# Kernel tuning notes

Hardware: AMD Instinct MI355X
Metric: run time of the kernel (lower is better)

The kernel has to match this reference:

```python
import jax, jax.numpy as jnp
import numpy as np

CHAR_EMB = 30
CHAR_HID = 100  # bidirectional -> 50 per direction
HID = CHAR_HID // 2
VOCAB = 100
B, S, T = 64, 256, 16


def setup_inputs() -> dict:
    key = jax.random.key(0)
    ks = jax.random.split(key, 10)
    char_ids = jax.random.randint(ks[0], (B, S, T), 0, VOCAB, dtype=jnp.int64)
    scale = np.sqrt(3.0 / CHAR_EMB)
    emb = jax.random.uniform(ks[1], (VOCAB, CHAR_EMB), minval=-scale, maxval=scale, dtype=jnp.float32)
    # torch LSTM param layout: w_ih [4H, in], w_hh [4H, H], gate order i,f,g,o
    k = 1.0 / np.sqrt(HID)
    def u(kk, shape):
        return jax.random.uniform(kk, shape, minval=-k, maxval=k, dtype=jnp.float32)
    return {
        "char_ids": char_ids,
        "emb": emb,
        "w_ih_f": u(ks[2], (4 * HID, CHAR_EMB)), "w_hh_f": u(ks[3], (4 * HID, HID)),
        "b_ih_f": u(ks[4], (4 * HID,)), "b_hh_f": u(ks[5], (4 * HID,)),
        "w_ih_r": u(ks[6], (4 * HID, CHAR_EMB)), "w_hh_r": u(ks[7], (4 * HID, HID)),
        "b_ih_r": u(ks[8], (4 * HID,)), "b_hh_r": u(ks[9], (4 * HID,)),
    }


def _lstm_scan(x, w_ih, w_hh, b_ih, b_hh):
    # x: [N, T, E] -> outputs ys [T, N, H], final h [N, H]
    N = x.shape[0]
    xw = jnp.einsum('nte,ge->ntg', x, w_ih) + (b_ih + b_hh)  # [N, T, 4H]
    xw = jnp.transpose(xw, (1, 0, 2))  # [T, N, 4H]

    def step(carry, xt):
        h, c = carry
        gates = xt + h @ w_hh.T
        i, f, g, o = jnp.split(gates, 4, axis=-1)
        i = jax.nn.sigmoid(i); f = jax.nn.sigmoid(f)
        g = jnp.tanh(g); o = jax.nn.sigmoid(o)
        c = f * c + i * g
        h = o * jnp.tanh(c)
        return (h, c), h

    h0 = jnp.zeros((N, HID), x.dtype)
    (hT, _), ys = jax.lax.scan(step, (h0, h0), xw)
    return ys, hT


def reference(char_ids, emb, w_ih_f, w_hh_f, b_ih_f, b_hh_f,
              w_ih_r, w_hh_r, b_ih_r, b_hh_r):
    b, s, t = char_ids.shape
    ids = char_ids.reshape(b * s, t)                 # [N, T]
    lengths = (ids != 0).sum(axis=1)                 # ragged lengths (pad id 0)
    x = emb[ids]                                     # [N, T, E]; dropout = identity (eval)

    # forward direction: need hidden at position lengths-1
    ys_f, _ = _lstm_scan(x, w_ih_f, w_hh_f, b_ih_f, b_hh_f)   # [T, N, H]
    ys_f = jnp.transpose(ys_f, (1, 0, 2))                      # [N, T, H]
    idx = jnp.maximum(lengths - 1, 0)[:, None, None]           # guard all-pad rows
    h_fwd = jnp.take_along_axis(ys_f, idx, axis=1)[:, 0, :]    # [N, H]

    # backward direction: output at t=0 == final carry of reversed scan
    _, h_bwd = _lstm_scan(x[:, ::-1, :], w_ih_r, w_hh_r, b_ih_r, b_hh_r)  # [N, H]

    out = jnp.concatenate([h_fwd, h_bwd], axis=-1)   # [N, 2H]
    return out.reshape(b, s, CHAR_HID)
```

## Files before the change

### kernel.cpp

```cpp
#include <hip/hip_runtime.h>

#define T 16
#define E 30
#define H 50
#define VOCAB 100
#define ROWS 208
#define K1 1.44269504089f
#define K2 2.88539008178f
#define NTILE 13

typedef _Float16 v8hf __attribute__((ext_vector_type(8)));
typedef float v4f __attribute__((ext_vector_type(4)));

extern "C" __device__ float __ocml_native_exp2_f32(float);
__device__ __forceinline__ float e2(float x)   { return __ocml_native_exp2_f32(x); }
__device__ __forceinline__ float rcpf(float x) { return __builtin_amdgcn_rcpf(x); }

__global__ void build_tbl(const float* __restrict__ emb,
                          const float* __restrict__ w_ih,
                          const float* __restrict__ b_ih,
                          const float* __restrict__ b_hh,
                          float* __restrict__ tbl) {
    int idx = blockIdx.x * blockDim.x + threadIdx.x;
    if (idx >= VOCAB * ROWS) return;
    int v = idx / ROWS, r = idx % ROWS;
    float s = 0.f;
    if (r < 4 * H) {
        int orig = (r & 3) * H + (r >> 2);
        s = b_ih[orig] + b_hh[orig];
        const float* er = emb + v * E;
        const float* wr = w_ih + orig * E;
#pragma unroll
        for (int e = 0; e < E; ++e) s += er[e] * wr[e];
        s *= ((r & 3) == 2) ? K2 : -K1;
    }
    tbl[idx] = s;
}

__global__ __launch_bounds__(256, 2) void lstm_mfma(
    const int* __restrict__ ids,
    const float* __restrict__ tbl,
    const float* __restrict__ whh_f,
    const float* __restrict__ whh_r,
    float* __restrict__ out)
{
    __shared__ _Float16 hbuf[4][2][64][8];

    const int tid = threadIdx.x;
    const int lane = tid & 63;
    const int wave = tid >> 6;
    const int l15 = lane & 15;
    const int lg = lane >> 4;
    const int b = blockIdx.x;
    const int dir = b >> 8;
    const int seq = (b & 255) * 64 + wave * 16 + l15;

    const float* __restrict__ whh = dir ? whh_r : whh_f;
    const float* __restrict__ tb  = tbl + dir * (VOCAB * ROWS);
    const int* __restrict__ myids = ids + seq * T;

    _Float16* hb = &hbuf[wave][0][0][0];

    {
        int4* z = (int4*)hb;
        int4 zero; zero.x = zero.y = zero.z = zero.w = 0;
        z[lane] = zero;
        z[lane + 64] = zero;
    }

    int capt;
    {
        const int4* q = (const int4*)myids;
        int4 a0 = q[0], a1 = q[1], a2 = q[2], a3 = q[3];
        int len = (a0.x != 0) + (a0.y != 0) + (a0.z != 0) + (a0.w != 0)
                + (a1.x != 0) + (a1.y != 0) + (a1.z != 0) + (a1.w != 0)
                + (a2.x != 0) + (a2.y != 0) + (a2.z != 0) + (a2.w != 0)
                + (a3.x != 0) + (a3.y != 0) + (a3.z != 0) + (a3.w != 0);
        capt = dir ? (T - 1) : ((len > 1) ? (len - 1) : 0);
    }

    v8hf afrag[NTILE][2];
#pragma unroll
    for (int i = 0; i < NTILE; ++i) {
        const int r = i * 16 + l15;
        const bool vr = (r < 4 * H);
        const int orig = vr ? ((r & 3) * H + (r >> 2)) : 0;
        const float sc = ((r & 3) == 2) ? K2 : -K1;
#pragma unroll
        for (int kh = 0; kh < 2; ++kh) {
            v8hf af;
#pragma unroll
            for (int j = 0; j < 8; ++j) {
                const int k = kh * 32 + lg * 8 + j;
                af[j] = (_Float16)((vr && k < H) ? sc * whh[orig * H + k] : 0.f);
            }
            afrag[i][kh] = af;
        }
    }

    unsigned wa[NTILE];
#pragma unroll
    for (int i = 0; i < NTILE; ++i) {
        const int u = i * 4 + lg;
        wa[i] = ((u >> 5) << 9) + (((u & 31) >> 3) << 7) + (l15 << 3) + (u & 7);
    }
    const _Float16* rb0 = hb + lane * 8;
    const _Float16* rb1 = hb + 512 + lane * 8;

    float cs[NTILE], hcap[NTILE];
#pragma unroll
    for (int i = 0; i < NTILE; ++i) { cs[i] = 0.f; hcap[i] = 0.f; }

    v4f tv[NTILE];
    {
        const int id0 = myids[dir ? (T - 1) : 0];
        const float* __restrict__ trow = tb + id0 * ROWS;
#pragma unroll
        for (int i = 0; i < NTILE; ++i)
            tv[i] = *(const v4f*)(trow + i * 16 + lg * 4);
    }

#pragma unroll 1
    for (int t = 0; t < T; ++t) {
        int tn = dir ? (T - 2 - t) : (t + 1);
        if (t == T - 1) tn = dir ? 0 : (T - 1);
        const int id_next = myids[tn];
        const float* __restrict__ trow_n = tb + id_next * ROWS;

        v8hf bh0 = *(const v8hf*)rb0;
        v8hf bh1 = *(const v8hf*)rb1;

        const bool cap = (t == capt);

#pragma unroll
        for (int i = 0; i < NTILE; ++i) {
            v4f c = __builtin_amdgcn_mfma_f32_16x16x32_f16(afrag[i][0], bh0, tv[i], 0, 0, 0);
            c = __builtin_amdgcn_mfma_f32_16x16x32_f16(afrag[i][1], bh1, c, 0, 0, 0);
            tv[i] = *(const v4f*)(trow_n + i * 16 + lg * 4);

            float ei = e2(c[0]);
            float ef = e2(c[1]);
            float eg = e2(c[2]);
            float eo = e2(c[3]);
            float ai  = 1.f + ei;
            float bf  = 1.f + ef;
            float gp  = eg + 1.f;
            float gm2 = fmaf(K2, eg, -K2);
            float num = fmaf(cs[i] * ai, gp, gm2 * bf);
            float rD  = rcpf(ai * bf * gp);
            float cn  = num * rD;
            cs[i] = cn;
            float ec  = e2(cn);
            float em  = ec - 1.f;
            float ep  = ec + 1.f;
            float eo1 = 1.f + eo;
            float hn  = em * rcpf(eo1 * ep);

            if (i < 12 || lg < 2) {
                hb[wa[i]] = (_Float16)hn;
                hcap[i] = cap ? hn : hcap[i];
            }
        }
    }

#pragma unroll
    for (int i = 0; i < NTILE; ++i) {
        const int u = i * 4 + lg;
        if (u < H) out[seq * 100 + dir * H + u] = hcap[i];
    }
}

extern "C" void kernel_launch(void* const* d_in, const int* in_sizes, int n_in,
                              void* d_out, int out_size, void* d_ws, size_t ws_size,
                              hipStream_t stream) {
    const int*   char_ids = (const int*)d_in[0];
    const float* emb      = (const float*)d_in[1];
    const float* w_ih_f   = (const float*)d_in[2];
    const float* w_hh_f   = (const float*)d_in[3];
    const float* b_ih_f   = (const float*)d_in[4];
    const float* b_hh_f   = (const float*)d_in[5];
    const float* w_ih_r   = (const float*)d_in[6];
    const float* w_hh_r   = (const float*)d_in[7];
    const float* b_ih_r   = (const float*)d_in[8];
    const float* b_hh_r   = (const float*)d_in[9];
    float* out = (float*)d_out;
    float* tbl = (float*)d_ws;

    const int nt = VOCAB * ROWS;
    build_tbl<<<(nt + 255) / 256, 256, 0, stream>>>(emb, w_ih_f, b_ih_f, b_hh_f, tbl);
    build_tbl<<<(nt + 255) / 256, 256, 0, stream>>>(emb, w_ih_r, b_ih_r, b_hh_r, tbl + nt);
    lstm_mfma<<<512, 256, 0, stream>>>(char_ids, tbl, w_hh_f, w_hh_r, out);
}
```

Measured before the change: 65.67 us.

## Split LSTM gate tiles across two waves with double-buffered LDS hidden state

Each 16-sequence group is now processed by two waves, one owning 7 gate tiles and the other 6, instead of a single wave owning all 13. The hidden state is exchanged through a double-buffered LDS area with a barrier every timestep, and the launch grows to 2048 blocks of 128 threads. This shortens the serial per-step MFMA and transcendental chain per wave and increases the number of waves available for latency hiding. In exchange it adds a per-step block barrier, and the captured output is now stored directly inside the loop rather than kept in registers until the end.

```diff
diff --git a/kernel.cpp b/kernel.cpp
--- a/kernel.cpp
+++ b/kernel.cpp
@@ -7,7 +7,6 @@
 #define ROWS 208
 #define K1 1.44269504089f
 #define K2 2.88539008178f
-#define NTILE 13
 
 typedef _Float16 v8hf __attribute__((ext_vector_type(8)));
 typedef float v4f __attribute__((ext_vector_type(4)));
@@ -37,52 +36,19 @@
     tbl[idx] = s;
 }
 
-__global__ __launch_bounds__(256, 2) void lstm_mfma(
-    const int* __restrict__ ids,
-    const float* __restrict__ tbl,
-    const float* __restrict__ whh_f,
-    const float* __restrict__ whh_r,
-    float* __restrict__ out)
+template<int RT0, int NT>
+__device__ __forceinline__ void run_tiles(
+    const float* __restrict__ whh, const float* __restrict__ tb,
+    const int* __restrict__ myids, _Float16* __restrict__ hb,
+    float* __restrict__ out, int seq, int dir, int capt, int lane)
 {
-    __shared__ _Float16 hbuf[4][2][64][8];
-
-    const int tid = threadIdx.x;
-    const int lane = tid & 63;
-    const int wave = tid >> 6;
     const int l15 = lane & 15;
     const int lg = lane >> 4;
-    const int b = blockIdx.x;
-    const int dir = b >> 8;
-    const int seq = (b & 255) * 64 + wave * 16 + l15;
 
-    const float* __restrict__ whh = dir ? whh_r : whh_f;
-    const float* __restrict__ tb  = tbl + dir * (VOCAB * ROWS);
-    const int* __restrict__ myids = ids + seq * T;
-
-    _Float16* hb = &hbuf[wave][0][0][0];
-
-    {
-        int4* z = (int4*)hb;
-        int4 zero; zero.x = zero.y = zero.z = zero.w = 0;
-        z[lane] = zero;
-        z[lane + 64] = zero;
-    }
-
-    int capt;
-    {
-        const int4* q = (const int4*)myids;
-        int4 a0 = q[0], a1 = q[1], a2 = q[2], a3 = q[3];
-        int len = (a0.x != 0) + (a0.y != 0) + (a0.z != 0) + (a0.w != 0)
-                + (a1.x != 0) + (a1.y != 0) + (a1.z != 0) + (a1.w != 0)
-                + (a2.x != 0) + (a2.y != 0) + (a2.z != 0) + (a2.w != 0)
-                + (a3.x != 0) + (a3.y != 0) + (a3.z != 0) + (a3.w != 0);
-        capt = dir ? (T - 1) : ((len > 1) ? (len - 1) : 0);
-    }
-
-    v8hf afrag[NTILE][2];
+    v8hf afrag[NT][2];
 #pragma unroll
-    for (int i = 0; i < NTILE; ++i) {
-        const int r = i * 16 + l15;
+    for (int i = 0; i < NT; ++i) {
+        const int r = (RT0 + i) * 16 + l15;
         const bool vr = (r < 4 * H);
         const int orig = vr ? ((r & 3) * H + (r >> 2)) : 0;
         const float sc = ((r & 3) == 2) ? K2 : -K1;
@@ -98,45 +64,45 @@
         }
     }
 
-    unsigned wa[NTILE];
+    unsigned wa[NT];
 #pragma unroll
-    for (int i = 0; i < NTILE; ++i) {
-        const int u = i * 4 + lg;
+    for (int i = 0; i < NT; ++i) {
+        const int u = (RT0 + i) * 4 + lg;
         wa[i] = ((u >> 5) << 9) + (((u & 31) >> 3) << 7) + (l15 << 3) + (u & 7);
     }
-    const _Float16* rb0 = hb + lane * 8;
-    const _Float16* rb1 = hb + 512 + lane * 8;
 
-    float cs[NTILE], hcap[NTILE];
+    float cs[NT];
 #pragma unroll
-    for (int i = 0; i < NTILE; ++i) { cs[i] = 0.f; hcap[i] = 0.f; }
+    for (int i = 0; i < NT; ++i) cs[i] = 0.f;
 
-    v4f tv[NTILE];
+    v4f tv[NT];
     {
         const int id0 = myids[dir ? (T - 1) : 0];
         const float* __restrict__ trow = tb + id0 * ROWS;
 #pragma unroll
-        for (int i = 0; i < NTILE; ++i)
-            tv[i] = *(const v4f*)(trow + i * 16 + lg * 4);
+        for (int i = 0; i < NT; ++i)
+            tv[i] = *(const v4f*)(trow + (RT0 + i) * 16 + lg * 4);
     }
 
 #pragma unroll 1
     for (int t = 0; t < T; ++t) {
+        const int cur = t & 1, nxt = cur ^ 1;
         int tn = dir ? (T - 2 - t) : (t + 1);
         if (t == T - 1) tn = dir ? 0 : (T - 1);
         const int id_next = myids[tn];
         const float* __restrict__ trow_n = tb + id_next * ROWS;
 
-        v8hf bh0 = *(const v8hf*)rb0;
-        v8hf bh1 = *(const v8hf*)rb1;
+        v8hf bh0 = *(const v8hf*)(hb + cur * 1024 + lane * 8);
+        v8hf bh1 = *(const v8hf*)(hb + cur * 1024 + 512 + lane * 8);
 
+        _Float16* wb = hb + nxt * 1024;
         const bool cap = (t == capt);
 
 #pragma unroll
-        for (int i = 0; i < NTILE; ++i) {
+        for (int i = 0; i < NT; ++i) {
             v4f c = __builtin_amdgcn_mfma_f32_16x16x32_f16(afrag[i][0], bh0, tv[i], 0, 0, 0);
             c = __builtin_amdgcn_mfma_f32_16x16x32_f16(afrag[i][1], bh1, c, 0, 0, 0);
-            tv[i] = *(const v4f*)(trow_n + i * 16 + lg * 4);
+            tv[i] = *(const v4f*)(trow_n + (RT0 + i) * 16 + lg * 4);
 
             float ei = e2(c[0]);
             float ef = e2(c[1]);
@@ -151,23 +117,63 @@
             float cn  = num * rD;
             cs[i] = cn;
             float ec  = e2(cn);
-            float em  = ec - 1.f;
-            float ep  = ec + 1.f;
-            float eo1 = 1.f + eo;
-            float hn  = em * rcpf(eo1 * ep);
+            float hn  = (ec - 1.f) * rcpf((1.f + eo) * (ec + 1.f));
 
-            if (i < 12 || lg < 2) {
-                hb[wa[i]] = (_Float16)hn;
-                hcap[i] = cap ? hn : hcap[i];
+            if (RT0 + i < 12 || lg < 2) {
+                wb[wa[i]] = (_Float16)hn;
+                if (cap) out[seq * 100 + dir * H + (RT0 + i) * 4 + lg] = hn;
             }
         }
+
+        asm volatile("s_waitcnt lgkmcnt(0)" ::: "memory");
+        __builtin_amdgcn_s_barrier();
+        asm volatile("" ::: "memory");
+    }
+}
+
+__global__ __launch_bounds__(128, 4) void lstm_mfma(
+    const int* __restrict__ ids,
+    const float* __restrict__ tbl,
+    const float* __restrict__ whh_f,
+    const float* __restrict__ whh_r,
+    float* __restrict__ out)
+{
+    __shared__ _Float16 hbuf[2][2][64][8];
+
+    const int tid = threadIdx.x;
+    const int lane = tid & 63;
+    const int wv = tid >> 6;
+    const int l15 = lane & 15;
+    const int b = blockIdx.x;
+    const int dir = b >> 10;
+    const int seq = (b & 1023) * 16 + l15;
+
+    const float* __restrict__ whh = dir ? whh_r : whh_f;
+    const float* __restrict__ tb  = tbl + dir * (VOCAB * ROWS);
+    const int* __restrict__ myids = ids + seq * T;
+
+    {
+        int* hz = (int*)&hbuf[0][0][0][0];
+#pragma unroll
+        for (int i = tid; i < 1024; i += 128) hz[i] = 0;
     }
 
-#pragma unroll
-    for (int i = 0; i < NTILE; ++i) {
-        const int u = i * 4 + lg;
-        if (u < H) out[seq * 100 + dir * H + u] = hcap[i];
+    int capt;
+    {
+        const int4* q = (const int4*)myids;
+        int4 a0 = q[0], a1 = q[1], a2 = q[2], a3 = q[3];
+        int len = (a0.x != 0) + (a0.y != 0) + (a0.z != 0) + (a0.w != 0)
+                + (a1.x != 0) + (a1.y != 0) + (a1.z != 0) + (a1.w != 0)
+                + (a2.x != 0) + (a2.y != 0) + (a2.z != 0) + (a2.w != 0)
+                + (a3.x != 0) + (a3.y != 0) + (a3.z != 0) + (a3.w != 0);
+        capt = dir ? (T - 1) : ((len > 1) ? (len - 1) : 0);
     }
+
+    __syncthreads();
+
+    _Float16* hb = &hbuf[0][0][0][0];
+    if (wv == 0) run_tiles<0, 7>(whh, tb, myids, hb, out, seq, dir, capt, lane);
+    else         run_tiles<7, 6>(whh, tb, myids, hb, out, seq, dir, capt, lane);
 }
 
 extern "C" void kernel_launch(void* const* d_in, const int* in_sizes, int n_in,
@@ -189,5 +195,5 @@
     const int nt = VOCAB * ROWS;
     build_tbl<<<(nt + 255) / 256, 256, 0, stream>>>(emb, w_ih_f, b_ih_f, b_hh_f, tbl);
     build_tbl<<<(nt + 255) / 256, 256, 0, stream>>>(emb, w_ih_r, b_ih_r, b_hh_r, tbl + nt);
-    lstm_mfma<<<512, 256, 0, stream>>>(char_ids, tbl, w_hh_f, w_hh_r, out);
+    lstm_mfma<<<2048, 128, 0, stream>>>(char_ids, tbl, w_hh_f, w_hh_r, out);
 }
```

Result: slower. 70.28 us (+7.0%).

## Permute hidden-unit layout so recurrent h stays in registers, dropping LDS round-trip

Applied to the files above, without the earlier changes.

The gate rows are remapped so each lane group owns 13 consecutive hidden units, laid out so that the MFMA output layout directly matches the B-operand layout for the next step. The hidden state can therefore be packed into fp16 registers without the per-step shared-memory write and read. The input table build and the W_hh fragment loading are changed to the same permutation. Captured outputs are now written to global memory inside the loop when the capture step hits, which removes the hcap registers.

```diff
diff --git a/kernel.cpp b/kernel.cpp
--- a/kernel.cpp
+++ b/kernel.cpp
@@ -24,15 +24,18 @@
     int idx = blockIdx.x * blockDim.x + threadIdx.x;
     if (idx >= VOCAB * ROWS) return;
     int v = idx / ROWS, r = idx % ROWS;
+    int tile = r >> 4, rho = r & 15;
+    int lgc = rho >> 2, gate = rho & 3;
+    int u = lgc * 13 + tile;
     float s = 0.f;
-    if (r < 4 * H) {
-        int orig = (r & 3) * H + (r >> 2);
+    if (u < H) {
+        int orig = gate * H + u;
         s = b_ih[orig] + b_hh[orig];
         const float* er = emb + v * E;
         const float* wr = w_ih + orig * E;
 #pragma unroll
         for (int e = 0; e < E; ++e) s += er[e] * wr[e];
-        s *= ((r & 3) == 2) ? K2 : -K1;
+        s *= (gate == 2) ? K2 : -K1;
     }
     tbl[idx] = s;
 }
@@ -44,8 +47,6 @@
     const float* __restrict__ whh_r,
     float* __restrict__ out)
 {
-    __shared__ _Float16 hbuf[4][2][64][8];
-
     const int tid = threadIdx.x;
     const int lane = tid & 63;
     const int wave = tid >> 6;
@@ -59,15 +60,6 @@
     const float* __restrict__ tb  = tbl + dir * (VOCAB * ROWS);
     const int* __restrict__ myids = ids + seq * T;
 
-    _Float16* hb = &hbuf[wave][0][0][0];
-
-    {
-        int4* z = (int4*)hb;
-        int4 zero; zero.x = zero.y = zero.z = zero.w = 0;
-        z[lane] = zero;
-        z[lane + 64] = zero;
-    }
-
     int capt;
     {
         const int4* q = (const int4*)myids;
@@ -79,37 +71,35 @@
         capt = dir ? (T - 1) : ((len > 1) ? (len - 1) : 0);
     }
 
+    const int gate = l15 & 3;
+    const int rbase = (l15 >> 2) * 13;
+    const float sc = (gate == 2) ? K2 : -K1;
     v8hf afrag[NTILE][2];
 #pragma unroll
     for (int i = 0; i < NTILE; ++i) {
-        const int r = i * 16 + l15;
-        const bool vr = (r < 4 * H);
-        const int orig = vr ? ((r & 3) * H + (r >> 2)) : 0;
-        const float sc = ((r & 3) == 2) ? K2 : -K1;
+        const int urow = rbase + i;
+        const bool vrow = (urow < H);
+        const int worow = (gate * H + (vrow ? urow : 0)) * H;
 #pragma unroll
         for (int kh = 0; kh < 2; ++kh) {
             v8hf af;
 #pragma unroll
             for (int j = 0; j < 8; ++j) {
-                const int k = kh * 32 + lg * 8 + j;
-                af[j] = (_Float16)((vr && k < H) ? sc * whh[orig * H + k] : 0.f);
+                const int m = kh * 8 + j;
+                const int ucol = lg * 13 + m;
+                const bool vcol = (m < NTILE) && (ucol < H);
+                af[j] = (_Float16)((vrow && vcol) ? sc * whh[worow + ucol] : 0.f);
             }
             afrag[i][kh] = af;
         }
     }
 
-    unsigned wa[NTILE];
+    float cs[NTILE];
 #pragma unroll
-    for (int i = 0; i < NTILE; ++i) {
-        const int u = i * 4 + lg;
-        wa[i] = ((u >> 5) << 9) + (((u & 31) >> 3) << 7) + (l15 << 3) + (u & 7);
-    }
-    const _Float16* rb0 = hb + lane * 8;
-    const _Float16* rb1 = hb + 512 + lane * 8;
+    for (int i = 0; i < NTILE; ++i) cs[i] = 0.f;
 
-    float cs[NTILE], hcap[NTILE];
-#pragma unroll
-    for (int i = 0; i < NTILE; ++i) { cs[i] = 0.f; hcap[i] = 0.f; }
+    v8hf b0 = (v8hf)(_Float16)0.f;
+    v8hf b1 = (v8hf)(_Float16)0.f;
 
     v4f tv[NTILE];
     {
@@ -126,16 +116,13 @@
         if (t == T - 1) tn = dir ? 0 : (T - 1);
         const int id_next = myids[tn];
         const float* __restrict__ trow_n = tb + id_next * ROWS;
-
-        v8hf bh0 = *(const v8hf*)rb0;
-        v8hf bh1 = *(const v8hf*)rb1;
-
         const bool cap = (t == capt);
 
+        float hn[NTILE];
 #pragma unroll
         for (int i = 0; i < NTILE; ++i) {
-            v4f c = __builtin_amdgcn_mfma_f32_16x16x32_f16(afrag[i][0], bh0, tv[i], 0, 0, 0);
-            c = __builtin_amdgcn_mfma_f32_16x16x32_f16(afrag[i][1], bh1, c, 0, 0, 0);
+            v4f c = __builtin_amdgcn_mfma_f32_16x16x32_f16(afrag[i][0], b0, tv[i], 0, 0, 0);
+            c = __builtin_amdgcn_mfma_f32_16x16x32_f16(afrag[i][1], b1, c, 0, 0, 0);
             tv[i] = *(const v4f*)(trow_n + i * 16 + lg * 4);
 
             float ei = e2(c[0]);
@@ -151,22 +138,21 @@
             float cn  = num * rD;
             cs[i] = cn;
             float ec  = e2(cn);
-            float em  = ec - 1.f;
-            float ep  = ec + 1.f;
-            float eo1 = 1.f + eo;
-            float hn  = em * rcpf(eo1 * ep);
+            float h   = (ec - 1.f) * rcpf((1.f + eo) * (ec + 1.f));
 
-            if (i < 12 || lg < 2) {
-                hb[wa[i]] = (_Float16)hn;
-                hcap[i] = cap ? hn : hcap[i];
-            }
+            if (i >= 11) h = (lg < 3) ? h : 0.f;
+            hn[i] = h;
+            if (cap && (i < 11 || lg < 3))
+                out[seq * 100 + dir * H + lg * NTILE + i] = h;
         }
-    }
 
+        v8hf nb0, nb1;
 #pragma unroll
-    for (int i = 0; i < NTILE; ++i) {
-        const int u = i * 4 + lg;
-        if (u < H) out[seq * 100 + dir * H + u] = hcap[i];
+        for (int j = 0; j < 8; ++j) nb0[j] = (_Float16)hn[j];
+#pragma unroll
+        for (int j = 0; j < 5; ++j) nb1[j] = (_Float16)hn[8 + j];
+        nb1[5] = (_Float16)0.f; nb1[6] = (_Float16)0.f; nb1[7] = (_Float16)0.f;
+        b0 = nb0; b1 = nb1;
     }
 }
 
```

Result: no change. 66.10 us (+0.6%).
